# Kernel optimization log

Measured on AMD Instinct MI355X. Metric: run time of the kernel, lower is better.

Reference implementation:

```python
import jax, jax.numpy as jnp
import numpy as np

N_NODES = 100000
N_EDGES = 3200000
F_IN = 16
F_HID = 32


def _gcn_conv(x, row, col, edge_w, W, b, num_nodes):
    # PyG GCNConv: gcn_norm with add_self_loops=True (fill_value=1.0),
    # symmetric normalization, then x @ W.T aggregated over edges, + bias.
    loop = jnp.arange(num_nodes)
    r = jnp.concatenate([row, loop])
    c = jnp.concatenate([col, loop])
    ew = jnp.concatenate([edge_w, jnp.ones((num_nodes,), dtype=edge_w.dtype)])
    deg = jax.ops.segment_sum(ew, c, num_segments=num_nodes)
    dis = jnp.where(deg > 0, jax.lax.rsqrt(deg), 0.0)
    norm = dis[r] * ew * dis[c]  # [E+N]
    xw = x @ W.T                 # [N, out]
    msg = xw[r] * norm[:, None]  # gather + scale
    out = jax.ops.segment_sum(msg, c, num_segments=num_nodes)
    return out + b


def setup_inputs() -> dict:
    key = jax.random.key(0)
    ks = jax.random.split(key, 8)
    x = jax.random.normal(ks[0], (N_NODES, F_IN), dtype=jnp.float32)
    edge_index = jax.random.randint(ks[1], (2, N_EDGES), 0, N_NODES, dtype=jnp.int64)
    edge_w = jax.random.uniform(ks[2], (N_EDGES,), dtype=jnp.float32)
    W1 = jax.random.normal(ks[3], (F_HID, F_IN), dtype=jnp.float32) * 0.1
    b1 = jax.random.normal(ks[4], (F_HID,), dtype=jnp.float32) * 0.1
    W2 = jax.random.normal(ks[5], (F_IN, F_HID), dtype=jnp.float32) * 0.1
    b2 = jax.random.normal(ks[6], (F_IN,), dtype=jnp.float32) * 0.1
    return {"x": x, "edge_index": edge_index, "edge_w": edge_w,
            "W1": W1, "b1": b1, "W2": W2, "b2": b2, "num_nodes": N_NODES}


def reference(x, edge_index, edge_w, W1, b1, W2, b2, num_nodes):
    row, col = edge_index[0], edge_index[1]
    h = _gcn_conv(x, row, col, edge_w, W1, b1, num_nodes)
    h = jax.nn.relu(h)
    out = _gcn_conv(h, row, col, edge_w, W2, b2, num_nodes)
    return out
```

## Files before the change

kernel.cpp:

```cpp
#include <hip/hip_runtime.h>
#include <hip/hip_fp16.h>
#include <cstdint>


#define BS 256
#define CHUNKS 256

__device__ __forceinline__ int2 nt_load_edge(const int2* p) {
    long long v = __builtin_nontemporal_load((const long long*)p);
    int2 r;
    r.x = (int)(v & 0xFFFFFFFFll);
    r.y = (int)(v >> 32);
    return r;
}

__device__ __forceinline__ float4 load_h4(const __half* p) {
    uint2 u = *(const uint2*)p;
    __half2 p0 = *(__half2*)&u.x;
    __half2 p1 = *(__half2*)&u.y;
    float2 f0 = __half22float2(p0);
    float2 f1 = __half22float2(p1);
    float4 r;
    r.x = f0.x; r.y = f0.y; r.z = f1.x; r.w = f1.y;
    return r;
}

__global__ __launch_bounds__(1024) void hist_kernel(
        const int* __restrict__ col, int* __restrict__ part,
        int E, int nbuck, int per) {
    extern __shared__ int sh[];
    for (int t = threadIdx.x; t < nbuck; t += blockDim.x) sh[t] = 0;
    __syncthreads();
    int lo = blockIdx.x * per, hi = min(E, lo + per);
    for (int e = lo + threadIdx.x; e < hi; e += blockDim.x)
        atomicAdd(&sh[col[e] >> 8], 1);
    __syncthreads();
    for (int t = threadIdx.x; t < nbuck; t += blockDim.x)
        part[(size_t)blockIdx.x * nbuck + t] = sh[t];
}

__global__ void colscan_kernel(const int* __restrict__ part, int* __restrict__ base,
                               int* __restrict__ tot, int nbuck) {
    int b = blockIdx.x;
    if (b >= nbuck) return;
    int lane = threadIdx.x;
    int off = 0;
    for (int g = 0; g < CHUNKS; g += 64) {
        int c = g + lane;
        int v = part[(size_t)c * nbuck + b];
        int s = v;
        #pragma unroll
        for (int d = 1; d < 64; d <<= 1) {
            int t = __shfl_up(s, d);
            if (lane >= d) s += t;
        }
        base[(size_t)c * nbuck + b] = off + (s - v);
        off += __shfl(s, 63);
    }
    if (lane == 0) tot[b] = off;
}

__global__ void scan1_kernel(const int* __restrict__ cnt, int* __restrict__ excl,
                             int* __restrict__ bsum, int n) {
    __shared__ int s[256];
    int tid = threadIdx.x;
    int i = blockIdx.x * 256 + tid;
    int v = (i < n) ? cnt[i] : 0;
    s[tid] = v;
    __syncthreads();
    for (int off = 1; off < 256; off <<= 1) {
        int t = (tid >= off) ? s[tid - off] : 0;
        __syncthreads();
        s[tid] += t;
        __syncthreads();
    }
    if (i < n) excl[i] = s[tid] - v;
    if (tid == 255) bsum[blockIdx.x] = s[255];
}

__global__ void scan2_kernel(int* __restrict__ bsum, int nb) {
    __shared__ int s[512];
    int tid = threadIdx.x;
    int v = (tid < nb) ? bsum[tid] : 0;
    s[tid] = v;
    __syncthreads();
    for (int off = 1; off < 512; off <<= 1) {
        int t = (tid >= off) ? s[tid - off] : 0;
        __syncthreads();
        s[tid] += t;
        __syncthreads();
    }
    if (tid < nb) bsum[tid] = s[tid] - v;
}

__global__ void scan3_kernel(int* __restrict__ excl, const int* __restrict__ bsum,
                             int n, int E) {
    int i = blockIdx.x * 256 + threadIdx.x;
    if (i < n) excl[i] += bsum[i >> 8];
    else if (i == n) excl[n] = E;
}

__global__ __launch_bounds__(1024) void place_kernel(
        const int* __restrict__ row, const int* __restrict__ col,
        const float* __restrict__ ew,
        const int* __restrict__ start, const int* __restrict__ base,
        int2* __restrict__ rw, int E, int nbuck, int per) {
    extern __shared__ int sh[];
    int* lbase = sh;
    int* cnt2  = sh + nbuck;
    int c = blockIdx.x;
    for (int t = threadIdx.x; t < nbuck; t += blockDim.x) {
        lbase[t] = start[t] + base[(size_t)c * nbuck + t];
        cnt2[t] = 0;
    }
    __syncthreads();
    int lo = c * per, hi = min(E, lo + per);
    for (int e = lo + threadIdx.x; e < hi; e += blockDim.x) {
        int cc = col[e];
        int b = cc >> 8;
        int p = lbase[b] + atomicAdd(&cnt2[b], 1);
        int2 v;
        v.x = row[e] | ((cc & 255) << 20);
        v.y = __float_as_int(ew[e]);
        rw[p] = v;
    }
}

__global__ __launch_bounds__(512) void nodesort_kernel(
        const int2* __restrict__ rw, const int* __restrict__ start,
        int2* __restrict__ rw2, int* __restrict__ ptr,
        float* __restrict__ dis, int N, int E, int nbuck) {
    __shared__ int cnt[BS];
    __shared__ float fdeg[BS];
    __shared__ int fill[BS];
    __shared__ int stmp[BS];
    int b = blockIdx.x, tid = threadIdx.x;
    for (int t = tid; t < BS; t += 512) { cnt[t] = 0; fdeg[t] = 0.f; }
    __syncthreads();
    int s0 = start[b], s1 = start[b + 1];
    for (int e = s0 + tid; e < s1; e += 512) {
        int2 v = rw[e];
        int cl = v.x >> 20;
        atomicAdd(&cnt[cl], 1);
        atomicAdd(&fdeg[cl], __int_as_float(v.y));
    }
    __syncthreads();

    int myc = 0;
    if (tid < BS) { myc = cnt[tid]; stmp[tid] = myc; }
    __syncthreads();
    for (int off = 1; off < BS; off <<= 1) {
        int t = 0;
        if (tid < BS && tid >= off) t = stmp[tid - off];
        __syncthreads();
        if (tid < BS) stmp[tid] += t;
        __syncthreads();
    }
    if (tid < BS) {
        int excl = stmp[tid] - myc;
        ptr[b * BS + tid] = s0 + excl;
        fill[tid] = excl;
        int node = b * BS + tid;
        if (node < N) dis[node] = rsqrtf(fdeg[tid] + 1.0f);
    }
    __syncthreads();

    for (int e = s0 + tid; e < s1; e += 512) {
        int2 v = rw[e];
        int cl = v.x >> 20;
        int p = s0 + atomicAdd(&fill[cl], 1);
        int2 o;
        o.x = (v.x & 0xFFFFF) << 5;
        o.y = v.y;
        rw2[p] = o;
    }
    if (b == 0 && tid == 0) ptr[nbuck * BS] = E;
}

__global__ void xsc_kernel(const float* __restrict__ x, const float* __restrict__ dis,
                           __half* __restrict__ xsc, int N) {
    int i = blockIdx.x * 256 + threadIdx.x;
    if (i >= N) return;
    float d = dis[i];
    const float4* xr = (const float4*)(x + (size_t)i * 16);
    __half2 h[8];
#pragma unroll
    for (int k = 0; k < 4; ++k) {
        float4 v = xr[k];
        h[2*k]   = __floats2half2_rn(v.x * d, v.y * d);
        h[2*k+1] = __floats2half2_rn(v.z * d, v.w * d);
    }
    uint4* dst = (uint4*)(xsc + (size_t)i * 16);
    dst[0] = *(uint4*)&h[0];
    dst[1] = *(uint4*)&h[4];
}

template <int FINAL>
__global__ __launch_bounds__(256) void gather_kernel(
        const int* __restrict__ ptr, const int2* __restrict__ rw2,
        const __half* __restrict__ src, const float* __restrict__ dis,
        const float* __restrict__ b2, float* __restrict__ dst, int N) {
    int tid  = threadIdx.x;
    int wave = tid >> 6;
    int lane = tid & 63;
    int g = lane >> 4;
    int s = (lane >> 2) & 3;
    int q = lane & 3;
    int node = (blockIdx.x * 4 + wave) * 4 + g;
    if (node >= N) return;
    int s0 = ptr[node], s1 = ptr[node + 1];

    const char* srcb = (const char*)src;
    float4 a0 = {0.f, 0.f, 0.f, 0.f}, a1 = {0.f, 0.f, 0.f, 0.f};
    int e = s0 + s;
    for (; e + 4 < s1; e += 8) {
        int2 v0 = nt_load_edge(&rw2[e]);
        int2 v1 = nt_load_edge(&rw2[e + 4]);
        float4 x0 = load_h4((const __half*)(srcb + v0.x) + q * 4);
        float4 x1 = load_h4((const __half*)(srcb + v1.x) + q * 4);
        float w0 = __int_as_float(v0.y), w1 = __int_as_float(v1.y);
        a0.x += w0 * x0.x; a0.y += w0 * x0.y; a0.z += w0 * x0.z; a0.w += w0 * x0.w;
        a1.x += w1 * x1.x; a1.y += w1 * x1.y; a1.z += w1 * x1.z; a1.w += w1 * x1.w;
    }
    if (e < s1) {
        int2 v0 = nt_load_edge(&rw2[e]);
        float4 x0 = load_h4((const __half*)(srcb + v0.x) + q * 4);
        float w0 = __int_as_float(v0.y);
        a0.x += w0 * x0.x; a0.y += w0 * x0.y; a0.z += w0 * x0.z; a0.w += w0 * x0.w;
    }
    a0.x += a1.x; a0.y += a1.y; a0.z += a1.z; a0.w += a1.w;
#pragma unroll
    for (int m = 4; m <= 8; m <<= 1) {
        a0.x += __shfl_xor(a0.x, m);
        a0.y += __shfl_xor(a0.y, m);
        a0.z += __shfl_xor(a0.z, m);
        a0.w += __shfl_xor(a0.w, m);
    }

    if (s == 0) {
        float d = dis[node];
        float4 self = load_h4((const __half*)(srcb + ((size_t)node << 5)) + q * 4);
        float4 o;
        o.x = d * (a0.x + self.x);
        o.y = d * (a0.y + self.y);
        o.z = d * (a0.z + self.z);
        o.w = d * (a0.w + self.w);
        if (FINAL) {
            float4 bb = *(const float4*)(b2 + q * 4);
            o.x += bb.x; o.y += bb.y; o.z += bb.z; o.w += bb.w;
        }
        *(float4*)(dst + (size_t)node * 16 + q * 4) = o;
    }
}

__global__ __launch_bounds__(256) void mlp_kernel(
        const float* __restrict__ t, const float* __restrict__ dis,
        const float* __restrict__ W1, const float* __restrict__ b1,
        const float* __restrict__ W2, __half* __restrict__ xs2, int N) {
    __shared__ float sW1[512];
    __shared__ float sW2[512];
    __shared__ float sb1[32];
    for (int k = threadIdx.x; k < 512; k += 256) {
        sW1[k] = W1[k];
        sW2[k] = W2[k];
    }
    if (threadIdx.x < 32) sb1[threadIdx.x] = b1[threadIdx.x];
    __syncthreads();
    int i = blockIdx.x * 256 + threadIdx.x;
    if (i >= N) return;

    float tr[16];
#pragma unroll
    for (int k = 0; k < 4; ++k) {
        float4 v = ((const float4*)(t + (size_t)i * 16))[k];
        tr[4*k+0] = v.x; tr[4*k+1] = v.y; tr[4*k+2] = v.z; tr[4*k+3] = v.w;
    }
    float h[32];
#pragma unroll
    for (int o = 0; o < 32; ++o) {
        float acc = sb1[o];
#pragma unroll
        for (int k = 0; k < 16; ++k) acc += tr[k] * sW1[o * 16 + k];
        h[o] = fmaxf(acc, 0.f);
    }
    float d = dis[i];
    float o16[16];
#pragma unroll
    for (int o = 0; o < 16; ++o) {
        float acc = 0.f;
#pragma unroll
        for (int k = 0; k < 32; ++k) acc += h[k] * sW2[o * 32 + k];
        o16[o] = acc * d;
    }
    __half2 hh[8];
#pragma unroll
    for (int k = 0; k < 8; ++k) hh[k] = __floats2half2_rn(o16[2*k], o16[2*k+1]);
    uint4* dst = (uint4*)(xs2 + (size_t)i * 16);
    dst[0] = *(uint4*)&hh[0];
    dst[1] = *(uint4*)&hh[4];
}

extern "C" void kernel_launch(void* const* d_in, const int* in_sizes, int n_in,
                              void* d_out, int out_size, void* d_ws, size_t ws_size,
                              hipStream_t stream) {
    const float* x  = (const float*)d_in[0];
    const int*   ei = (const int*)d_in[1];
    const float* ew = (const float*)d_in[2];
    const float* W1 = (const float*)d_in[3];
    const float* b1 = (const float*)d_in[4];
    const float* W2 = (const float*)d_in[5];
    const float* b2 = (const float*)d_in[6];
    float* out = (float*)d_out;

    const int N = in_sizes[0] / 16;
    const int E = in_sizes[2];
    const int* row = ei;
    const int* col = ei + E;

    const int nbuck = (N + BS - 1) / BS;
    const int per   = (E + CHUNKS - 1) / CHUNKS;
    const int nb    = (nbuck + 255) / 256;

    float*  ws    = (float*)d_ws;
    int2*   rw2   = (int2*)ws;
    int2*   rw    = (int2*)(ws + (size_t)2 * E);
    __half* xsc   = (__half*)(ws + (size_t)2 * E);
    float*  tbuf  = ws + (size_t)2 * E + (size_t)8 * N;
    __half* xs2   = (__half*)(ws + (size_t)2 * E + (size_t)24 * N);
    float*  dis   = ws + (size_t)4 * E;
    int*    ptr   = (int*)(dis + N);
    int*    part  = ptr + (size_t)BS * nbuck + 1;
    int*    base  = part + (size_t)CHUNKS * nbuck;
    int*    tot   = base + (size_t)CHUNKS * nbuck;
    int*    start = tot + nbuck;
    int*    bsum  = start + nbuck + 1;

    hist_kernel<<<CHUNKS, 1024, nbuck * 4, stream>>>(col, part, E, nbuck, per);
    colscan_kernel<<<nbuck, 64, 0, stream>>>(part, base, tot, nbuck);
    scan1_kernel<<<nb, 256, 0, stream>>>(tot, start, bsum, nbuck);
    scan2_kernel<<<1, 512, 0, stream>>>(bsum, nb);
    scan3_kernel<<<(nbuck + 256) / 256 + 1, 256, 0, stream>>>(start, bsum, nbuck, E);
    place_kernel<<<CHUNKS, 1024, 2 * nbuck * 4, stream>>>(row, col, ew, start, base, rw, E, nbuck, per);
    nodesort_kernel<<<nbuck, 512, 0, stream>>>(rw, start, rw2, ptr, dis, N, E, nbuck);

    xsc_kernel<<<(N + 255) / 256, 256, 0, stream>>>(x, dis, xsc, N);
    {
        int gblocks = (N + 15) / 16;
        gather_kernel<0><<<gblocks, 256, 0, stream>>>(ptr, rw2, xsc, dis, b2, tbuf, N);
        mlp_kernel<<<(N + 255) / 256, 256, 0, stream>>>(tbuf, dis, W1, b1, W2, xs2, N);
        gather_kernel<1><<<gblocks, 256, 0, stream>>>(ptr, rw2, xs2, dis, b2, out, N);
    }
}
```

Baseline: 177.9 us.

## Split per-bucket node sort into three kernels over sub-slices; unroll place loop

Replaces the single nodesort kernel (one 512-thread block per 256-node bucket) with three kernels. The first counts per-slice histograms across S=4 sub-slices per bucket, the second scans the counts and computes per-slice offsets and degrees, and the third scatters edges using those offsets. The goal is more blocks and more parallelism for the histogram and scatter passes, since there are only about 391 buckets. The place kernel's loop is also unrolled by 4 to expose more memory-level parallelism, at the cost of two extra launches and extra global scratch traffic.

```diff
diff --git a/kernel.cpp b/kernel.cpp
--- a/kernel.cpp
+++ b/kernel.cpp
@@ -5,6 +5,7 @@
 
 #define BS 256
 #define CHUNKS 256
+#define S 4
 
 __device__ __forceinline__ int2 nt_load_edge(const int2* p) {
     long long v = __builtin_nontemporal_load((const long long*)p);
@@ -115,7 +116,32 @@
     }
     __syncthreads();
     int lo = c * per, hi = min(E, lo + per);
-    for (int e = lo + threadIdx.x; e < hi; e += blockDim.x) {
+    const int stride = blockDim.x;
+    int e = lo + threadIdx.x;
+    for (; e + 3 * stride < hi; e += 4 * stride) {
+        int cc[4], rr[4];
+        float w[4];
+#pragma unroll
+        for (int k = 0; k < 4; ++k) {
+            cc[k] = col[e + k * stride];
+            rr[k] = row[e + k * stride];
+            w[k]  = ew[e + k * stride];
+        }
+        int p[4];
+#pragma unroll
+        for (int k = 0; k < 4; ++k) {
+            int b = cc[k] >> 8;
+            p[k] = lbase[b] + atomicAdd(&cnt2[b], 1);
+        }
+#pragma unroll
+        for (int k = 0; k < 4; ++k) {
+            int2 v;
+            v.x = rr[k] | ((cc[k] & 255) << 20);
+            v.y = __float_as_int(w[k]);
+            rw[p[k]] = v;
+        }
+    }
+    for (; e < hi; e += stride) {
         int cc = col[e];
         int b = cc >> 8;
         int p = lbase[b] + atomicAdd(&cnt2[b], 1);
@@ -126,55 +152,90 @@
     }
 }
 
-__global__ __launch_bounds__(512) void nodesort_kernel(
+__global__ __launch_bounds__(256) void nsA_kernel(
         const int2* __restrict__ rw, const int* __restrict__ start,
-        int2* __restrict__ rw2, int* __restrict__ ptr,
-        float* __restrict__ dis, int N, int E, int nbuck) {
+        int* __restrict__ scnt, float* __restrict__ sdeg, int nbuck) {
     __shared__ int cnt[BS];
     __shared__ float fdeg[BS];
-    __shared__ int fill[BS];
-    __shared__ int stmp[BS];
-    int b = blockIdx.x, tid = threadIdx.x;
-    for (int t = tid; t < BS; t += 512) { cnt[t] = 0; fdeg[t] = 0.f; }
+    int b = blockIdx.x / S, sl = blockIdx.x % S;
+    int tid = threadIdx.x;
+    cnt[tid] = 0; fdeg[tid] = 0.f;
     __syncthreads();
     int s0 = start[b], s1 = start[b + 1];
-    for (int e = s0 + tid; e < s1; e += 512) {
+    int len = s1 - s0;
+    int lo = s0 + (int)(((long long)len * sl) / S);
+    int hi = s0 + (int)(((long long)len * (sl + 1)) / S);
+    for (int e = lo + tid; e < hi; e += 256) {
         int2 v = rw[e];
         int cl = v.x >> 20;
         atomicAdd(&cnt[cl], 1);
         atomicAdd(&fdeg[cl], __int_as_float(v.y));
     }
     __syncthreads();
-
-    int myc = 0;
-    if (tid < BS) { myc = cnt[tid]; stmp[tid] = myc; }
+    size_t o = (size_t)blockIdx.x * BS + tid;
+    scnt[o] = cnt[tid];
+    sdeg[o] = fdeg[tid];
+}
+
+__global__ __launch_bounds__(256) void nsB_kernel(
+        const int* __restrict__ start, int* __restrict__ scnt,
+        const float* __restrict__ sdeg, int* __restrict__ ptr,
+        float* __restrict__ dis, int N, int E, int nbuck) {
+    __shared__ int stmp[BS];
+    int b = blockIdx.x, tid = threadIdx.x;
+    int s0 = start[b];
+    int c[S];
+    float deg = 0.f;
+    int tot = 0;
+#pragma unroll
+    for (int sl = 0; sl < S; ++sl) {
+        size_t o = (size_t)(b * S + sl) * BS + tid;
+        c[sl] = scnt[o];
+        tot += c[sl];
+        deg += sdeg[o];
+    }
+    stmp[tid] = tot;
     __syncthreads();
     for (int off = 1; off < BS; off <<= 1) {
-        int t = 0;
-        if (tid < BS && tid >= off) t = stmp[tid - off];
-        __syncthreads();
-        if (tid < BS) stmp[tid] += t;
-        __syncthreads();
-    }
-    if (tid < BS) {
-        int excl = stmp[tid] - myc;
-        ptr[b * BS + tid] = s0 + excl;
-        fill[tid] = excl;
-        int node = b * BS + tid;
-        if (node < N) dis[node] = rsqrtf(fdeg[tid] + 1.0f);
-    }
-    __syncthreads();
-
-    for (int e = s0 + tid; e < s1; e += 512) {
+        int t = (tid >= off) ? stmp[tid - off] : 0;
+        __syncthreads();
+        stmp[tid] += t;
+        __syncthreads();
+    }
+    int excl = stmp[tid] - tot;
+    int node = b * BS + tid;
+    ptr[node] = s0 + excl;
+    if (node < N) dis[node] = rsqrtf(deg + 1.0f);
+    int acc = s0 + excl;
+#pragma unroll
+    for (int sl = 0; sl < S; ++sl) {
+        scnt[(size_t)(b * S + sl) * BS + tid] = acc;
+        acc += c[sl];
+    }
+    if (b == 0 && tid == 0) ptr[nbuck * BS] = E;
+}
+
+__global__ __launch_bounds__(256) void nsC_kernel(
+        const int2* __restrict__ rw, const int* __restrict__ start,
+        const int* __restrict__ scnt, int2* __restrict__ rw2, int nbuck) {
+    __shared__ int fill[BS];
+    int b = blockIdx.x / S, sl = blockIdx.x % S;
+    int tid = threadIdx.x;
+    fill[tid] = scnt[(size_t)blockIdx.x * BS + tid];
+    __syncthreads();
+    int s0 = start[b], s1 = start[b + 1];
+    int len = s1 - s0;
+    int lo = s0 + (int)(((long long)len * sl) / S);
+    int hi = s0 + (int)(((long long)len * (sl + 1)) / S);
+    for (int e = lo + tid; e < hi; e += 256) {
         int2 v = rw[e];
         int cl = v.x >> 20;
-        int p = s0 + atomicAdd(&fill[cl], 1);
+        int p = atomicAdd(&fill[cl], 1);
         int2 o;
         o.x = (v.x & 0xFFFFF) << 5;
         o.y = v.y;
         rw2[p] = o;
     }
-    if (b == 0 && tid == 0) ptr[nbuck * BS] = E;
 }
 
 __global__ void xsc_kernel(const float* __restrict__ x, const float* __restrict__ dis,
@@ -334,6 +395,8 @@
     int*    tot   = base + (size_t)CHUNKS * nbuck;
     int*    start = tot + nbuck;
     int*    bsum  = start + nbuck + 1;
+    int*    scnt  = bsum + 512;
+    float*  sdeg  = (float*)(scnt + (size_t)nbuck * S * BS);
 
     hist_kernel<<<CHUNKS, 1024, nbuck * 4, stream>>>(col, part, E, nbuck, per);
     colscan_kernel<<<nbuck, 64, 0, stream>>>(part, base, tot, nbuck);
@@ -341,7 +404,10 @@
     scan2_kernel<<<1, 512, 0, stream>>>(bsum, nb);
     scan3_kernel<<<(nbuck + 256) / 256 + 1, 256, 0, stream>>>(start, bsum, nbuck, E);
     place_kernel<<<CHUNKS, 1024, 2 * nbuck * 4, stream>>>(row, col, ew, start, base, rw, E, nbuck, per);
-    nodesort_kernel<<<nbuck, 512, 0, stream>>>(rw, start, rw2, ptr, dis, N, E, nbuck);
+
+    nsA_kernel<<<nbuck * S, 256, 0, stream>>>(rw, start, scnt, sdeg, nbuck);
+    nsB_kernel<<<nbuck, 256, 0, stream>>>(start, scnt, sdeg, ptr, dis, N, E, nbuck);
+    nsC_kernel<<<nbuck * S, 256, 0, stream>>>(rw, start, scnt, rw2, nbuck);
 
     xsc_kernel<<<(N + 255) / 256, 256, 0, stream>>>(x, dis, xsc, N);
     {
```

Result: slower. 193.6 us (+8.8%).
